# Optimization experiments

Hardware: AMD Instinct MI355X
Metric: run time of the kernel (lower is better)

The kernel has to match this reference:

```python
import jax, jax.numpy as jnp
import numpy as np

N_NODES = 50000
N_EDGES = 200000
IN_DIM = 16
NODE_DIM = 64
EDGE_DIM = 16
HIDDEN = 256
NUM_LAYERS = 4  # 1 NNConv + 3 GINConv


def setup_inputs() -> dict:
    key = jax.random.key(0)
    ks = jax.random.split(key, 20)
    s = 0.05
    inp = {
        "x": jax.random.normal(ks[0], (N_NODES, IN_DIM), dtype=jnp.float32),
        "edge_index": jax.random.randint(ks[1], (2, N_EDGES), 0, N_NODES, dtype=jnp.int64),
        "edge_attr": jax.random.normal(ks[2], (N_EDGES, EDGE_DIM), dtype=jnp.float32),
        # edge-NN (per-edge weight generator): attr_dim -> 256 -> 1024 -> in*out, ELU after each
        "enn_w1": jax.random.normal(ks[3], (EDGE_DIM, 256), dtype=jnp.float32) * s,
        "enn_b1": jnp.zeros((256,), dtype=jnp.float32),
        "enn_w2": jax.random.normal(ks[4], (256, 1024), dtype=jnp.float32) * s,
        "enn_b2": jnp.zeros((1024,), dtype=jnp.float32),
        "enn_w3": jax.random.normal(ks[5], (1024, IN_DIM * NODE_DIM), dtype=jnp.float32) * s,
        "enn_b3": jnp.zeros((IN_DIM * NODE_DIM,), dtype=jnp.float32),
        # NNConv root weight + bias
        "root_w": jax.random.normal(ks[6], (IN_DIM, NODE_DIM), dtype=jnp.float32) * s,
        "root_b": jnp.zeros((NODE_DIM,), dtype=jnp.float32),
        # 3 GIN MLPs (stacked): node_dim -> hidden -> hidden -> node_dim
        "gin_w1": jax.random.normal(ks[7], (3, NODE_DIM, HIDDEN), dtype=jnp.float32) * s,
        "gin_b1": jnp.zeros((3, HIDDEN), dtype=jnp.float32),
        "gin_w2": jax.random.normal(ks[8], (3, HIDDEN, HIDDEN), dtype=jnp.float32) * s,
        "gin_b2": jnp.zeros((3, HIDDEN), dtype=jnp.float32),
        "gin_w3": jax.random.normal(ks[9], (3, HIDDEN, NODE_DIM), dtype=jnp.float32) * s,
        "gin_b3": jnp.zeros((3, NODE_DIM), dtype=jnp.float32),
    }
    return inp


def _elu(x):
    return jax.nn.elu(x)


def reference(x, edge_index, edge_attr,
              enn_w1, enn_b1, enn_w2, enn_b2, enn_w3, enn_b3,
              root_w, root_b,
              gin_w1, gin_b1, gin_w2, gin_b2, gin_w3, gin_b3):
    src = edge_index[0]  # x_j (message source)
    dst = edge_index[1]  # i (aggregation target)

    # ---- Layer 0: NNConv with per-edge MLP-generated weights ----
    h = _elu(edge_attr @ enn_w1 + enn_b1)
    h = _elu(h @ enn_w2 + enn_b2)
    w_e = _elu(h @ enn_w3 + enn_b3).reshape(-1, IN_DIM, NODE_DIM)  # [E, in, out]
    msg = jnp.einsum('ei,eio->eo', x[src], w_e)                    # [E, node_dim]
    agg = jax.ops.segment_sum(msg, dst, num_segments=N_NODES)     # scatter-add
    x_cur = x @ root_w + agg + root_b                              # [N, node_dim]
    node_emb = [x_cur]

    # ---- Layers 1..3: GINConv (eps=0) with 3-layer MLP ----
    for l in range(NUM_LAYERS - 1):
        x_in = _elu(x_cur)
        nbr = jax.ops.segment_sum(x_in[src], dst, num_segments=N_NODES)
        h = x_in + nbr  # (1 + eps) * x + sum_j x_j, eps = 0
        h = _elu(h @ gin_w1[l] + gin_b1[l])
        h = _elu(h @ gin_w2[l] + gin_b2[l])
        x_cur = h @ gin_w3[l] + gin_b3[l]
        node_emb.append(x_cur)

    return jnp.stack(node_emb, axis=2)  # [N, node_dim, num_layers]
```

## Files before the change

### kernel.cpp

```cpp
#include <hip/hip_runtime.h>
#include <hip/hip_bf16.h>


#define NN 50000
#define EE 200000

typedef unsigned short u16;
typedef __attribute__((ext_vector_type(8))) short frag8;
typedef __attribute__((ext_vector_type(4))) float f32x4;

__device__ __forceinline__ float bf2f(u16 u) {
    union { unsigned int i; float f; } v; v.i = ((unsigned int)u) << 16; return v.f;
}
__device__ __forceinline__ u16 f2bf(float f) {
    union { float f; unsigned int i; } v; v.f = f;
    return (u16)((v.i + 0x7fffu + ((v.i >> 16) & 1u)) >> 16);
}
__device__ __forceinline__ float eluf(float v) {
    return v > 0.f ? v : __expf(v) - 1.f;
}

__global__ void probe_f32(const u16* __restrict__ raw, int* __restrict__ cnt) {
    int t = threadIdx.x;
    int c = 0;
    for (int j = t; j < 1024; j += 256) {
        unsigned e = (raw[j] >> 7) & 0xFF;
        if (e >= 0xBF) c++;
    }
    if (c) atomicAdd(cnt, c);
}
__global__ void cvt_bf16(const void* __restrict__ src, u16* __restrict__ dst, long n,
                         const int* __restrict__ cnt) {
    long i = (long)blockIdx.x * 256 + threadIdx.x;
    if (i >= n) return;
    if (*cnt >= 8) dst[i] = f2bf(((const float*)src)[i]);
    else           dst[i] = ((const u16*)src)[i];
}

__global__ void detect_idx64(const unsigned long long* __restrict__ p, int* __restrict__ flag) {
    long t = (long)blockIdx.x * 256 + threadIdx.x;
    if (t < EE) {
        unsigned long long v = p[t];
        if (v >> 31) atomicOr(flag, 1);
    }
}
__global__ void convert_idx(const void* __restrict__ raw, const int* __restrict__ flag,
                            int* __restrict__ s_out, int* __restrict__ d_out) {
    long t = (long)blockIdx.x * 256 + threadIdx.x;
    if (t >= EE) return;
    if (*flag) {
        const int* q = (const int*)raw;
        s_out[t] = q[t];
        d_out[t] = q[EE + t];
    } else {
        const long long* q = (const long long*)raw;
        s_out[t] = (int)q[t];
        d_out[t] = (int)q[EE + t];
    }
}

__global__ void transpose_bf16(const u16* __restrict__ in, u16* __restrict__ out, int K, int N) {
    long idx = (long)blockIdx.x * 256 + threadIdx.x;
    if (idx < (long)K * N) {
        int k = (int)(idx / N);
        int n = (int)(idx % N);
        out[(long)n * K + k] = in[idx];
    }
}

__global__ void edge_mlp1(const u16* __restrict__ attr, const u16* __restrict__ w1,
                          const u16* __restrict__ b1, u16* __restrict__ h1, int ce) {
    __shared__ u16 sa[256];
    const int t = threadIdx.x;
    const int e0 = blockIdx.x * 16;
    const int cnt = min(16, ce - e0);
    sa[t] = (t < cnt * 16) ? attr[(long)e0 * 16 + t] : (u16)0;
    float w[16];
    #pragma unroll
    for (int i = 0; i < 16; ++i) w[i] = bf2f(w1[i * 256 + t]);
    const float bb = bf2f(b1[t]);
    __syncthreads();
    for (int e = 0; e < cnt; ++e) {
        float v = bb;
        #pragma unroll
        for (int i = 0; i < 16; ++i) v += bf2f(sa[e * 16 + i]) * w[i];
        h1[(long)(e0 + e) * 256 + t] = f2bf(eluf(v));
    }
}

__device__ __forceinline__ void stage_tile(const u16* g, long row_base, long max_row,
                                           int kstride, int k0, u16* s, int t) {
    int wave = t >> 6;
    #pragma unroll
    for (int j = 0; j < 2; ++j) {
        int c = t + 256 * j;
        long r = row_base + (c >> 2);
        if (r > max_row) r = max_row;
        const u16* gp = g + r * (long)kstride + k0 + (c & 3) * 8;
        __builtin_amdgcn_global_load_lds(
            (__attribute__((address_space(1))) void*)(void*)gp,
            (__attribute__((address_space(3))) void*)((char*)s + wave * 1024 + j * 4096),
            16, 0, 0);
    }
}

__global__ __launch_bounds__(256)
void gemm_bt_bias_elu(const u16* __restrict__ A, const u16* __restrict__ BT,
                      const u16* __restrict__ bias, u16* __restrict__ C,
                      int M, int K, int N, int mpx, int lognt) {
    const int bid = blockIdx.x;
    const int xcd = bid & 7;
    const int j = bid >> 3;
    const int m_idx = xcd * mpx + (j >> lognt);
    const int n_idx = j & ((1 << lognt) - 1);
    const int num_m = (M + 127) >> 7;
    if (m_idx >= num_m) return;

    __shared__ __align__(16) u16 sA[128 * 32];
    __shared__ __align__(16) u16 sB[128 * 32];
    const int t = threadIdx.x;
    const int lane = t & 63;
    const int wave = t >> 6;
    const int wr = wave >> 1, wc = wave & 1;
    const int quad = lane >> 4, l16 = lane & 15;
    const long m0 = (long)m_idx * 128;
    const int n0 = n_idx * 128;

    f32x4 acc[4][4];
    const f32x4 z4 = {0.f, 0.f, 0.f, 0.f};
    #pragma unroll
    for (int mi = 0; mi < 4; ++mi)
        #pragma unroll
        for (int ni = 0; ni < 4; ++ni)
            acc[mi][ni] = z4;

    for (int k0 = 0; k0 < K; k0 += 32) {
        stage_tile(A, m0, (long)M - 1, K, k0, sA, t);
        stage_tile(BT, n0, (long)N - 1, K, k0, sB, t);
        __syncthreads();
        frag8 af[4], bfv[4];
        #pragma unroll
        for (int mi = 0; mi < 4; ++mi)
            af[mi] = *(const frag8*)(sA + (wr * 64 + mi * 16 + l16) * 32 + quad * 8);
        #pragma unroll
        for (int ni = 0; ni < 4; ++ni)
            bfv[ni] = *(const frag8*)(sB + (wc * 64 + ni * 16 + l16) * 32 + quad * 8);
        #pragma unroll
        for (int mi = 0; mi < 4; ++mi)
            #pragma unroll
            for (int ni = 0; ni < 4; ++ni)
                acc[mi][ni] = __builtin_amdgcn_mfma_f32_16x16x32_bf16(af[mi], bfv[ni], acc[mi][ni], 0, 0, 0);
        __syncthreads();
    }

    #pragma unroll
    for (int mi = 0; mi < 4; ++mi) {
        #pragma unroll
        for (int r = 0; r < 4; ++r) {
            long row = m0 + wr * 64 + mi * 16 + quad * 4 + r;
            if (row < M) {
                #pragma unroll
                for (int ni = 0; ni < 4; ++ni) {
                    int col = n0 + wc * 64 + ni * 16 + l16;
                    float v = acc[mi][ni][r] + bf2f(bias[col]);
                    C[row * (long)N + col] = f2bf(eluf(v));
                }
            }
        }
    }
}

__global__ __launch_bounds__(256)
void gemm_bt_f32(const u16* __restrict__ A, const u16* __restrict__ BT,
                 const u16* __restrict__ bias, float* __restrict__ C,
                 int M, int K) {
    __shared__ __align__(16) u16 sA[256 * 32];
    __shared__ __align__(16) u16 sB[64 * 32];
    const int t = threadIdx.x;
    const int lane = t & 63;
    const int wave = t >> 6;
    const int quad = lane >> 4, l16 = lane & 15;
    const long m0 = (long)blockIdx.x * 256;

    f32x4 acc[4][4];
    const f32x4 z4 = {0.f, 0.f, 0.f, 0.f};
    #pragma unroll
    for (int mi = 0; mi < 4; ++mi)
        #pragma unroll
        for (int ni = 0; ni < 4; ++ni)
            acc[mi][ni] = z4;

    for (int k0 = 0; k0 < K; k0 += 32) {
        #pragma unroll
        for (int j = 0; j < 4; ++j) {
            int c = t + 256 * j;
            long r = m0 + (c >> 2);
            if (r > (long)M - 1) r = (long)M - 1;
            const u16* gp = A + r * (long)K + k0 + (c & 3) * 8;
            __builtin_amdgcn_global_load_lds(
                (__attribute__((address_space(1))) void*)(void*)gp,
                (__attribute__((address_space(3))) void*)((char*)sA + wave * 1024 + j * 4096),
                16, 0, 0);
        }
        {
            int c = t;
            const u16* gp = BT + (long)(c >> 2) * K + k0 + (c & 3) * 8;
            __builtin_amdgcn_global_load_lds(
                (__attribute__((address_space(1))) void*)(void*)gp,
                (__attribute__((address_space(3))) void*)((char*)sB + wave * 1024),
                16, 0, 0);
        }
        __syncthreads();
        frag8 af[4], bfv[4];
        #pragma unroll
        for (int mi = 0; mi < 4; ++mi)
            af[mi] = *(const frag8*)(sA + (wave * 64 + mi * 16 + l16) * 32 + quad * 8);
        #pragma unroll
        for (int ni = 0; ni < 4; ++ni)
            bfv[ni] = *(const frag8*)(sB + (ni * 16 + l16) * 32 + quad * 8);
        #pragma unroll
        for (int mi = 0; mi < 4; ++mi)
            #pragma unroll
            for (int ni = 0; ni < 4; ++ni)
                acc[mi][ni] = __builtin_amdgcn_mfma_f32_16x16x32_bf16(af[mi], bfv[ni], acc[mi][ni], 0, 0, 0);
        __syncthreads();
    }

    #pragma unroll
    for (int mi = 0; mi < 4; ++mi) {
        #pragma unroll
        for (int r = 0; r < 4; ++r) {
            long row = m0 + wave * 64 + mi * 16 + quad * 4 + r;
            if (row < M) {
                #pragma unroll
                for (int ni = 0; ni < 4; ++ni) {
                    int col = ni * 16 + l16;
                    C[row * 64 + col] = acc[mi][ni][r] + bf2f(bias[col]);
                }
            }
        }
    }
}

__global__ void nnconv_msg(const u16* __restrict__ we, const u16* __restrict__ x,
                           const int* __restrict__ src, const int* __restrict__ dst,
                           float* __restrict__ agg, int ce) {
    long idx = (long)blockIdx.x * 256 + threadIdx.x;
    if (idx >= (long)ce * 64) return;
    int o = (int)(idx & 63);
    long e = idx >> 6;
    const u16* wr = we + e * 1024;
    const u16* xr = x + (long)src[e] * 16;
    float v = 0.f;
    #pragma unroll
    for (int i = 0; i < 16; ++i)
        v += bf2f(xr[i]) * bf2f(wr[i * 64 + o]);
    atomicAdd(&agg[(long)dst[e] * 64 + o], v);
}

__global__ void add_root(const u16* __restrict__ x, const u16* __restrict__ rw,
                         const u16* __restrict__ rb, float* __restrict__ xcur) {
    long idx = (long)blockIdx.x * 256 + threadIdx.x;
    if (idx >= (long)NN * 64) return;
    int d = (int)(idx & 63);
    long n = idx >> 6;
    float v = bf2f(rb[d]);
    #pragma unroll
    for (int i = 0; i < 16; ++i)
        v += bf2f(x[n * 16 + i]) * bf2f(rw[i * 64 + d]);
    xcur[idx] += v;
}

__global__ void elu_bf16(const float* __restrict__ in, u16* __restrict__ o, long n) {
    long idx = (long)blockIdx.x * 256 + threadIdx.x;
    if (idx < n) o[idx] = f2bf(eluf(in[idx]));
}

__global__ void gin_scatter(const u16* __restrict__ xin, const int* __restrict__ src,
                            const int* __restrict__ dst, float* __restrict__ nbr) {
    long idx = (long)blockIdx.x * 256 + threadIdx.x;
    if (idx >= (long)EE * 64) return;
    int d = (int)(idx & 63);
    long e = idx >> 6;
    atomicAdd(&nbr[(long)dst[e] * 64 + d], bf2f(xin[(long)src[e] * 64 + d]));
}

__global__ void gin_combine(const u16* __restrict__ xin, const float* __restrict__ nbr,
                            u16* __restrict__ hin, long n) {
    long idx = (long)blockIdx.x * 256 + threadIdx.x;
    if (idx < n) hin[idx] = f2bf(bf2f(xin[idx]) + nbr[idx]);
}

__global__ void write_out(const float* __restrict__ e0, const float* __restrict__ e1,
                          const float* __restrict__ e2, const float* __restrict__ e3,
                          float* __restrict__ out) {
    long idx = (long)blockIdx.x * 256 + threadIdx.x;
    if (idx >= (long)NN * 64) return;
    float4 v = {e0[idx], e1[idx], e2[idx], e3[idx]};
    *(float4*)(out + idx * 4) = v;
}

extern "C" void kernel_launch(void* const* d_in, const int* in_sizes, int n_in,
                              void* d_out, int out_size, void* d_ws, size_t ws_size,
                              hipStream_t stream) {
    (void)in_sizes; (void)n_in; (void)out_size;
    const void* eidx = d_in[1];
    float* out = (float*)d_out;

    char* ws = (char*)d_ws;
    size_t off = 0;
    auto alloc = [&](size_t bytes) {
        char* p = ws + off;
        off += (bytes + 255) & ~(size_t)255;
        return p;
    };
    int* src32 = (int*)alloc((size_t)EE * 4);
    int* dst32 = (int*)alloc((size_t)EE * 4);
    int* flag  = (int*)alloc(256);
    int* cnt   = (int*)alloc(256);
    const int cv_idx[16] = {0, 2, 3, 4, 5, 6, 7, 8, 9, 10, 11, 12, 13, 14, 15, 16};
    const long cv_n[16]  = {800000, 3200000, 4096, 256, 262144, 1024, 1048576, 1024,
                            1024, 64, 49152, 768, 196608, 768, 49152, 192};
    u16* cv[16];
    for (int i = 0; i < 16; ++i) cv[i] = (u16*)alloc((size_t)cv_n[i] * 2);
    u16 *xc = cv[0], *eac = cv[1], *w1c = cv[2], *b1c = cv[3], *w2c = cv[4], *b2c = cv[5],
        *w3c = cv[6], *b3c = cv[7], *rwc = cv[8], *rbc = cv[9],
        *g1c = cv[10], *gb1c = cv[11], *g2c = cv[12], *gb2c = cv[13], *g3c = cv[14], *gb3c = cv[15];
    u16* w2t = (u16*)alloc((size_t)1024 * 256 * 2);
    u16* w3t = (u16*)alloc((size_t)1024 * 1024 * 2);
    u16* g1t = (u16*)alloc((size_t)3 * 256 * 64 * 2);
    u16* g2t = (u16*)alloc((size_t)3 * 256 * 256 * 2);
    u16* g3t = (u16*)alloc((size_t)3 * 64 * 256 * 2);
    float* emb[4];
    for (int l = 0; l < 4; ++l) emb[l] = (float*)alloc((size_t)NN * 64 * 4);
    float* agg = emb[0];
    char* scratch = (char*)alloc(0);
    size_t avail = (ws_size > off + 4096) ? (ws_size - off - 4096) : 0;

    long CE = (long)(avail / 4608) & ~127L;
    if (CE < 128) CE = 128;
    if (CE > 200064) CE = 200064;
    u16* h1c = (u16*)scratch;
    u16* h2c = (u16*)(scratch + (size_t)CE * 512);
    u16* wec = (u16*)(scratch + (size_t)CE * 2560);

    long gin_fixed = (long)NN * 64 * 4 + (long)NN * 64 * 2;
    long gin_avail = (long)avail - gin_fixed;
    if (gin_avail < 0) gin_avail = 0;
    long CN = (gin_avail / 1152) & ~255L;
    if (CN < 256) CN = 256;
    if (CN > 50176) CN = 50176;
    float* nbr = (float*)scratch;
    u16* xin   = (u16*)(scratch + (size_t)NN * 64 * 4);
    u16* hin   = (u16*)(scratch + gin_fixed);
    u16* hg1   = hin + (size_t)CN * 64;
    u16* hg2   = hg1 + (size_t)CN * 256;

    auto cdiv = [](long a, long b) { return (unsigned)((a + b - 1) / b); };

    hipMemsetAsync(cnt, 0, 4, stream);
    probe_f32<<<1, 256, 0, stream>>>((const u16*)d_in[0], cnt);
    for (int i = 0; i < 16; ++i)
        cvt_bf16<<<cdiv(cv_n[i], 256), 256, 0, stream>>>(d_in[cv_idx[i]], cv[i], cv_n[i], cnt);

    hipMemsetAsync(flag, 0, 4, stream);
    detect_idx64<<<cdiv(EE, 256), 256, 0, stream>>>((const unsigned long long*)eidx, flag);
    convert_idx<<<cdiv(EE, 256), 256, 0, stream>>>(eidx, flag, src32, dst32);

    transpose_bf16<<<cdiv(256 * 1024, 256), 256, 0, stream>>>(w2c, w2t, 256, 1024);
    transpose_bf16<<<cdiv(1024 * 1024, 256), 256, 0, stream>>>(w3c, w3t, 1024, 1024);
    for (int l = 0; l < 3; ++l) {
        transpose_bf16<<<cdiv(64 * 256, 256), 256, 0, stream>>>(g1c + l * 64 * 256, g1t + l * 256 * 64, 64, 256);
        transpose_bf16<<<cdiv(256 * 256, 256), 256, 0, stream>>>(g2c + l * 256 * 256, g2t + l * 256 * 256, 256, 256);
        transpose_bf16<<<cdiv(256 * 64, 256), 256, 0, stream>>>(g3c + l * 256 * 64, g3t + l * 64 * 256, 256, 64);
    }

    hipMemsetAsync(agg, 0, (size_t)NN * 64 * 4, stream);
    for (long e0 = 0; e0 < EE; e0 += CE) {
        int ce = (int)((EE - e0 < CE) ? (EE - e0) : CE);
        int mpx = cdiv(cdiv(ce, 128), 8);
        edge_mlp1<<<cdiv(ce, 16), 256, 0, stream>>>(eac + e0 * 16, w1c, b1c, h1c, ce);
        gemm_bt_bias_elu<<<8 * mpx * 8, 256, 0, stream>>>(h1c, w2t, b2c, h2c, ce, 256, 1024, mpx, 3);
        gemm_bt_bias_elu<<<8 * mpx * 8, 256, 0, stream>>>(h2c, w3t, b3c, wec, ce, 1024, 1024, mpx, 3);
        nnconv_msg<<<cdiv((long)ce * 64, 256), 256, 0, stream>>>(wec, xc, src32 + e0, dst32 + e0, agg, ce);
    }
    add_root<<<cdiv((long)NN * 64, 256), 256, 0, stream>>>(xc, rwc, rbc, agg);

    for (int l = 0; l < 3; ++l) {
        elu_bf16<<<cdiv((long)NN * 64, 256), 256, 0, stream>>>(emb[l], xin, (long)NN * 64);
        hipMemsetAsync(nbr, 0, (size_t)NN * 64 * 4, stream);
        gin_scatter<<<cdiv((long)EE * 64, 256), 256, 0, stream>>>(xin, src32, dst32, nbr);
        for (long n0 = 0; n0 < NN; n0 += CN) {
            int cn = (int)((NN - n0 < CN) ? (NN - n0) : CN);
            int mpx = cdiv(cdiv(cn, 128), 8);
            gin_combine<<<cdiv((long)cn * 64, 256), 256, 0, stream>>>(xin + n0 * 64, nbr + n0 * 64, hin, (long)cn * 64);
            gemm_bt_bias_elu<<<8 * mpx * 2, 256, 0, stream>>>(hin, g1t + l * 256 * 64, gb1c + l * 256, hg1, cn, 64, 256, mpx, 1);
            gemm_bt_bias_elu<<<8 * mpx * 2, 256, 0, stream>>>(hg1, g2t + l * 256 * 256, gb2c + l * 256, hg2, cn, 256, 256, mpx, 1);
            gemm_bt_f32<<<cdiv(cn, 256), 256, 0, stream>>>(hg2, g3t + l * 64 * 256, gb3c + l * 64, emb[l + 1] + n0 * 64, cn, 256);
        }
    }
    write_out<<<cdiv((long)NN * 64, 256), 256, 0, stream>>>(emb[0], emb[1], emb[2], emb[3], out);
}
```

Before: 1.629 ms.

## Fuse per-edge weight GEMM with NNConv message and scatter, swizzle LDS tiles

The final edge-MLP GEMM now computes the message contraction in its epilogue. Each 128-column tile covers two input channels; it is scaled by the gathered source feature, the two halves are combined through shared memory, and the result is atomically added into the aggregate. This removes the [E,1024] per-edge weight tensor's write and re-read and lets the edge chunk size grow. Separately, all GEMM LDS tiles use an XOR swizzle on the 16-byte column slot to reduce bank conflicts on fragment reads. In exchange there are now 8x more atomics per edge, one per N-tile, plus extra shared memory per block.

```diff
diff --git a/kernel.cpp b/kernel.cpp
--- a/kernel.cpp
+++ b/kernel.cpp
@@ -94,14 +94,19 @@
     #pragma unroll
     for (int j = 0; j < 2; ++j) {
         int c = t + 256 * j;
-        long r = row_base + (c >> 2);
+        int row = c >> 2;
+        int col = (c & 3) ^ (row & 3);
+        long r = row_base + row;
         if (r > max_row) r = max_row;
-        const u16* gp = g + r * (long)kstride + k0 + (c & 3) * 8;
+        const u16* gp = g + r * (long)kstride + k0 + col * 8;
         __builtin_amdgcn_global_load_lds(
             (__attribute__((address_space(1))) void*)(void*)gp,
             (__attribute__((address_space(3))) void*)((char*)s + wave * 1024 + j * 4096),
             16, 0, 0);
     }
+}
+__device__ __forceinline__ frag8 frag_read(const u16* s, int r, int quad) {
+    return *(const frag8*)(s + r * 32 + ((quad ^ (r & 3)) * 8));
 }
 
 __global__ __launch_bounds__(256)
@@ -141,10 +146,10 @@
         frag8 af[4], bfv[4];
         #pragma unroll
         for (int mi = 0; mi < 4; ++mi)
-            af[mi] = *(const frag8*)(sA + (wr * 64 + mi * 16 + l16) * 32 + quad * 8);
-        #pragma unroll
-        for (int ni = 0; ni < 4; ++ni)
-            bfv[ni] = *(const frag8*)(sB + (wc * 64 + ni * 16 + l16) * 32 + quad * 8);
+            af[mi] = frag_read(sA, wr * 64 + mi * 16 + l16, quad);
+        #pragma unroll
+        for (int ni = 0; ni < 4; ++ni)
+            bfv[ni] = frag_read(sB, wc * 64 + ni * 16 + l16, quad);
         #pragma unroll
         for (int mi = 0; mi < 4; ++mi)
             #pragma unroll
@@ -167,6 +172,103 @@
                 }
             }
         }
+    }
+}
+
+__global__ __launch_bounds__(256)
+void gemm_msg_f(const u16* __restrict__ A, const u16* __restrict__ BT,
+                const u16* __restrict__ bias, const u16* __restrict__ x,
+                const int* __restrict__ src, const int* __restrict__ dst,
+                float* __restrict__ agg, int M, int mpx) {
+    const int bid = blockIdx.x;
+    const int xcd = bid & 7;
+    const int jj = bid >> 3;
+    const int m_idx = xcd * mpx + (jj >> 3);
+    const int n_idx = jj & 7;
+    const int num_m = (M + 127) >> 7;
+    if (m_idx >= num_m) return;
+    const int K = 1024;
+
+    __shared__ __align__(16) u16 sA[128 * 32];
+    __shared__ __align__(16) u16 sB[128 * 32];
+    __shared__ float smsg[128 * 64];
+    const int t = threadIdx.x;
+    const int lane = t & 63;
+    const int wave = t >> 6;
+    const int wr = wave >> 1, wc = wave & 1;
+    const int quad = lane >> 4, l16 = lane & 15;
+    const long m0 = (long)m_idx * 128;
+    const int n0 = n_idx * 128;
+
+    f32x4 acc[4][4];
+    const f32x4 z4 = {0.f, 0.f, 0.f, 0.f};
+    #pragma unroll
+    for (int mi = 0; mi < 4; ++mi)
+        #pragma unroll
+        for (int ni = 0; ni < 4; ++ni)
+            acc[mi][ni] = z4;
+
+    for (int k0 = 0; k0 < K; k0 += 32) {
+        stage_tile(A, m0, (long)M - 1, K, k0, sA, t);
+        stage_tile(BT, n0, 1023, K, k0, sB, t);
+        __syncthreads();
+        frag8 af[4], bfv[4];
+        #pragma unroll
+        for (int mi = 0; mi < 4; ++mi)
+            af[mi] = frag_read(sA, wr * 64 + mi * 16 + l16, quad);
+        #pragma unroll
+        for (int ni = 0; ni < 4; ++ni)
+            bfv[ni] = frag_read(sB, wc * 64 + ni * 16 + l16, quad);
+        #pragma unroll
+        for (int mi = 0; mi < 4; ++mi)
+            #pragma unroll
+            for (int ni = 0; ni < 4; ++ni)
+                acc[mi][ni] = __builtin_amdgcn_mfma_f32_16x16x32_bf16(af[mi], bfv[ni], acc[mi][ni], 0, 0, 0);
+        __syncthreads();
+    }
+
+    const int i_this = (n0 >> 6) + wc;
+    float xv[4][4];
+    #pragma unroll
+    for (int mi = 0; mi < 4; ++mi) {
+        #pragma unroll
+        for (int r = 0; r < 4; ++r) {
+            long e = m0 + wr * 64 + mi * 16 + quad * 4 + r;
+            xv[mi][r] = (e < M) ? bf2f(x[(long)src[e] * 16 + i_this]) : 0.f;
+        }
+    }
+    if (wc == 0) {
+        #pragma unroll
+        for (int mi = 0; mi < 4; ++mi)
+            #pragma unroll
+            for (int r = 0; r < 4; ++r) {
+                int rl = wr * 64 + mi * 16 + quad * 4 + r;
+                #pragma unroll
+                for (int ni = 0; ni < 4; ++ni) {
+                    int cl = ni * 16 + l16;
+                    smsg[rl * 64 + cl] = eluf(acc[mi][ni][r] + bf2f(bias[n0 + cl])) * xv[mi][r];
+                }
+            }
+    }
+    __syncthreads();
+    if (wc == 1) {
+        #pragma unroll
+        for (int mi = 0; mi < 4; ++mi)
+            #pragma unroll
+            for (int r = 0; r < 4; ++r) {
+                long e = m0 + wr * 64 + mi * 16 + quad * 4 + r;
+                if (e < M) {
+                    int rl = wr * 64 + mi * 16 + quad * 4 + r;
+                    float* dp = agg + (long)dst[e] * 64;
+                    #pragma unroll
+                    for (int ni = 0; ni < 4; ++ni) {
+                        int cl = ni * 16 + l16;
+                        float v = eluf(acc[mi][ni][r] + bf2f(bias[n0 + 64 + cl])) * xv[mi][r]
+                                  + smsg[rl * 64 + cl];
+                        atomicAdd(dp + cl, v);
+                    }
+                }
+            }
     }
 }
 
@@ -194,9 +296,11 @@
         #pragma unroll
         for (int j = 0; j < 4; ++j) {
             int c = t + 256 * j;
-            long r = m0 + (c >> 2);
+            int row = c >> 2;
+            int col = (c & 3) ^ (row & 3);
+            long r = m0 + row;
             if (r > (long)M - 1) r = (long)M - 1;
-            const u16* gp = A + r * (long)K + k0 + (c & 3) * 8;
+            const u16* gp = A + r * (long)K + k0 + col * 8;
             __builtin_amdgcn_global_load_lds(
                 (__attribute__((address_space(1))) void*)(void*)gp,
                 (__attribute__((address_space(3))) void*)((char*)sA + wave * 1024 + j * 4096),
@@ -204,7 +308,9 @@
         }
         {
             int c = t;
-            const u16* gp = BT + (long)(c >> 2) * K + k0 + (c & 3) * 8;
+            int row = c >> 2;
+            int col = (c & 3) ^ (row & 3);
+            const u16* gp = BT + (long)row * K + k0 + col * 8;
             __builtin_amdgcn_global_load_lds(
                 (__attribute__((address_space(1))) void*)(void*)gp,
                 (__attribute__((address_space(3))) void*)((char*)sB + wave * 1024),
@@ -214,10 +320,10 @@
         frag8 af[4], bfv[4];
         #pragma unroll
         for (int mi = 0; mi < 4; ++mi)
-            af[mi] = *(const frag8*)(sA + (wave * 64 + mi * 16 + l16) * 32 + quad * 8);
-        #pragma unroll
-        for (int ni = 0; ni < 4; ++ni)
-            bfv[ni] = *(const frag8*)(sB + (ni * 16 + l16) * 32 + quad * 8);
+            af[mi] = frag_read(sA, wave * 64 + mi * 16 + l16, quad);
+        #pragma unroll
+        for (int ni = 0; ni < 4; ++ni)
+            bfv[ni] = frag_read(sB, ni * 16 + l16, quad);
         #pragma unroll
         for (int mi = 0; mi < 4; ++mi)
             #pragma unroll
@@ -240,22 +346,6 @@
             }
         }
     }
-}
-
-__global__ void nnconv_msg(const u16* __restrict__ we, const u16* __restrict__ x,
-                           const int* __restrict__ src, const int* __restrict__ dst,
-                           float* __restrict__ agg, int ce) {
-    long idx = (long)blockIdx.x * 256 + threadIdx.x;
-    if (idx >= (long)ce * 64) return;
-    int o = (int)(idx & 63);
-    long e = idx >> 6;
-    const u16* wr = we + e * 1024;
-    const u16* xr = x + (long)src[e] * 16;
-    float v = 0.f;
-    #pragma unroll
-    for (int i = 0; i < 16; ++i)
-        v += bf2f(xr[i]) * bf2f(wr[i * 64 + o]);
-    atomicAdd(&agg[(long)dst[e] * 64 + o], v);
 }
 
 __global__ void add_root(const u16* __restrict__ x, const u16* __restrict__ rw,
@@ -337,12 +427,11 @@
     char* scratch = (char*)alloc(0);
     size_t avail = (ws_size > off + 4096) ? (ws_size - off - 4096) : 0;
 
-    long CE = (long)(avail / 4608) & ~127L;
+    long CE = (long)(avail / 2560) & ~127L;
     if (CE < 128) CE = 128;
     if (CE > 200064) CE = 200064;
     u16* h1c = (u16*)scratch;
     u16* h2c = (u16*)(scratch + (size_t)CE * 512);
-    u16* wec = (u16*)(scratch + (size_t)CE * 2560);
 
     long gin_fixed = (long)NN * 64 * 4 + (long)NN * 64 * 2;
     long gin_avail = (long)avail - gin_fixed;
@@ -381,8 +470,7 @@
         int mpx = cdiv(cdiv(ce, 128), 8);
         edge_mlp1<<<cdiv(ce, 16), 256, 0, stream>>>(eac + e0 * 16, w1c, b1c, h1c, ce);
         gemm_bt_bias_elu<<<8 * mpx * 8, 256, 0, stream>>>(h1c, w2t, b2c, h2c, ce, 256, 1024, mpx, 3);
-        gemm_bt_bias_elu<<<8 * mpx * 8, 256, 0, stream>>>(h2c, w3t, b3c, wec, ce, 1024, 1024, mpx, 3);
-        nnconv_msg<<<cdiv((long)ce * 64, 256), 256, 0, stream>>>(wec, xc, src32 + e0, dst32 + e0, agg, ce);
+        gemm_msg_f<<<8 * mpx * 8, 256, 0, stream>>>(h2c, w3t, b3c, xc, src32 + e0, dst32 + e0, agg, ce, mpx);
     }
     add_root<<<cdiv((long)NN * 64, 256), 256, 0, stream>>>(xc, rwc, rbc, agg);
 
```

Measured after the change: 2.237 ms. +37.3%, slower.
